# Optimization experiments

Measured on AMD Instinct MI355X. Metric: run time of the kernel, lower is better.

Reference implementation:

```python
import jax, jax.numpy as jnp
import numpy as np

B, S, H, E = 2, 4096, 2048, 8


def setup_inputs() -> dict:
    key = jax.random.key(0)
    k1, k2, k3 = jax.random.split(key, 3)
    x = jax.random.normal(k1, (B, S, H), dtype=jnp.float32)
    w_router = jax.random.normal(k2, (E, H), dtype=jnp.float32) * (1.0 / np.sqrt(H))
    # nn.Linear weight layout: [out_features, in_features] per expert -> [E, H, H]
    w_experts = jax.random.normal(k3, (E, H, H), dtype=jnp.float32) * (1.0 / np.sqrt(H))
    return {"x": x, "w_router": w_router, "w_experts": w_experts}


def reference(x, w_router, w_experts):
    # router logits: x @ W_r^T  -> [B, S, E]
    logits = jnp.einsum('bsh,eh->bse', x, w_router)
    idx = jnp.argmax(logits, axis=-1)  # [B, S] top-1 expert per token
    # dense all-expert outputs (matches original which evaluates every expert):
    # expert_e(x) = x @ W_e^T -> [B, S, E, H]
    all_out = jnp.einsum('bsh,efh->bsef', x, w_experts)
    # masked sum over one-hot mask == gather of the selected expert output
    out = jnp.take_along_axis(all_out, idx[:, :, None, None], axis=2)[:, :, 0, :]
    return out
```

## Files before the change

### kernel.cpp

```cpp
#include <hip/hip_runtime.h>
#include <hip/hip_bf16.h>
#include <cstdint>

#define T_TOK 8192
#define H_DIM 2048
#define N_EXP 8
#define FLAGBIT 0x80000000u

typedef __attribute__((ext_vector_type(4))) float f32x4;
typedef __attribute__((ext_vector_type(8))) short bf16x8;

__device__ __forceinline__ unsigned short f2bf(float f) {
  unsigned int u = __builtin_bit_cast(unsigned int, f);
  u += 0x7fffu + ((u >> 16) & 1u);
  return (unsigned short)(u >> 16);
}

#define GLL(SRC, DST) __builtin_amdgcn_global_load_lds( \
    (const __attribute__((address_space(1))) void*)(SRC), \
    (__attribute__((address_space(3))) void*)(DST), 16, 0, 0)

__global__ __launch_bounds__(256, 4) void k_conv_a(const float* __restrict__ we,
                                                   unsigned short* __restrict__ wb) {
  const size_t tix = ((size_t)blockIdx.x * 256 + threadIdx.x) * 8;
  const size_t stride = (size_t)1024 * 256 * 8;
  f32x4 v[16];
#pragma unroll
  for (int it = 0; it < 8; ++it) {
    v[2 * it]     = *reinterpret_cast<const f32x4*>(we + tix + (size_t)it * stride);
    v[2 * it + 1] = *reinterpret_cast<const f32x4*>(we + tix + (size_t)it * stride + 4);
  }
#pragma unroll
  for (int it = 0; it < 8; ++it) {
    union { unsigned short h[8]; uint4 u; } r;
#pragma unroll
    for (int q = 0; q < 4; ++q) {
      r.h[q]     = f2bf(v[2 * it][q]);
      r.h[4 + q] = f2bf(v[2 * it + 1][q]);
    }
    *reinterpret_cast<uint4*>(wb + tix + (size_t)it * stride) = r.u;
  }
}

__global__ __launch_bounds__(256, 4) void k_conv_b(const float* __restrict__ we,
                                                   unsigned short* __restrict__ wb) {
  const size_t tix = ((size_t)blockIdx.x * 256 + threadIdx.x) * 8;
  const size_t stride = (size_t)1024 * 256 * 8;
#pragma unroll
  for (int it = 0; it < 8; ++it) {
    const f32x4 a = *reinterpret_cast<const f32x4*>(we + tix + (size_t)it * stride);
    const f32x4 b = *reinterpret_cast<const f32x4*>(we + tix + (size_t)it * stride + 4);
    union { unsigned short h[8]; uint4 u; } r;
#pragma unroll
    for (int q = 0; q < 4; ++q) { r.h[q] = f2bf(a[q]); r.h[4 + q] = f2bf(b[q]); }
    *reinterpret_cast<uint4*>(wb + tix + (size_t)it * stride) = r.u;
  }
}

__global__ __launch_bounds__(256, 2) void k_router(const float* __restrict__ x,
    const float* __restrict__ wr, unsigned short* __restrict__ xb,
    int* __restrict__ idx)
{
  const int wv = threadIdx.x >> 6, lane = threadIdx.x & 63;
  const int t0 = (blockIdx.x * 4 + wv) * 4;
  float acc[4][N_EXP];
#pragma unroll
  for (int tt = 0; tt < 4; ++tt)
#pragma unroll
    for (int e = 0; e < N_EXP; ++e) acc[tt][e] = 0.f;
#pragma unroll
  for (int c = 0; c < H_DIM / 256; ++c) {
    const int h = c * 256 + lane * 4;
    float4 wvv[N_EXP];
#pragma unroll
    for (int e = 0; e < N_EXP; ++e)
      wvv[e] = *reinterpret_cast<const float4*>(wr + e * H_DIM + h);
#pragma unroll
    for (int tt = 0; tt < 4; ++tt) {
      const float4 xv = *reinterpret_cast<const float4*>(x + (size_t)(t0 + tt) * H_DIM + h);
      ushort4 bv;
      bv.x = f2bf(xv.x); bv.y = f2bf(xv.y); bv.z = f2bf(xv.z); bv.w = f2bf(xv.w);
      *reinterpret_cast<ushort4*>(xb + (size_t)(t0 + tt) * H_DIM + h) = bv;
#pragma unroll
      for (int e = 0; e < N_EXP; ++e) {
        acc[tt][e] = fmaf(xv.x, wvv[e].x, acc[tt][e]);
        acc[tt][e] = fmaf(xv.y, wvv[e].y, acc[tt][e]);
        acc[tt][e] = fmaf(xv.z, wvv[e].z, acc[tt][e]);
        acc[tt][e] = fmaf(xv.w, wvv[e].w, acc[tt][e]);
      }
    }
  }
#pragma unroll
  for (int off = 32; off >= 1; off >>= 1)
#pragma unroll
    for (int tt = 0; tt < 4; ++tt)
#pragma unroll
      for (int e = 0; e < N_EXP; ++e) acc[tt][e] += __shfl_xor(acc[tt][e], off, 64);
  if (lane == 0) {
#pragma unroll
    for (int tt = 0; tt < 4; ++tt) {
      float best = acc[tt][0]; int be = 0;
#pragma unroll
      for (int e = 1; e < N_EXP; ++e) if (acc[tt][e] > best) { best = acc[tt][e]; be = e; }
      idx[t0 + tt] = be;
    }
  }
}

__global__ __launch_bounds__(1024) void k_sort(const int* __restrict__ idx,
    int* __restrict__ tlist, int* __restrict__ estar, int* __restrict__ mlo,
    int* __restrict__ mhi, int* __restrict__ rpos, int* __restrict__ rtile,
    int* __restrict__ rtc)
{
  __shared__ int wc[N_EXP][128];
  __shared__ int wbase[N_EXP][128];
  __shared__ int sTot[N_EXP];
  __shared__ int off[N_EXP + 1];
  __shared__ int sE[32], sCnt[N_EXP], sBase[N_EXP];
  const int tid = threadIdx.x, w = tid >> 6, l = tid & 63;
  int myE[8];
#pragma unroll
  for (int j = 0; j < 8; ++j) {
    myE[j] = idx[j * 1024 + tid];
#pragma unroll
    for (int e = 0; e < N_EXP; ++e) {
      const unsigned long long bm = __ballot(myE[j] == e);
      if (l == e) wc[e][j * 16 + w] = __popcll(bm);
    }
  }
  __syncthreads();
  if (tid < N_EXP) {
    int s = 0;
    for (int k = 0; k < 128; ++k) { wbase[tid][k] = s; s += wc[tid][k]; }
    sTot[tid] = s;
  }
  __syncthreads();
  if (tid == 0) {
    off[0] = 0;
    for (int e = 0; e < N_EXP; ++e) off[e + 1] = off[e] + sTot[e];
  }
  __syncthreads();
#pragma unroll
  for (int j = 0; j < 8; ++j) {
    int rank = 0;
#pragma unroll
    for (int e = 0; e < N_EXP; ++e) {
      const unsigned long long bm = __ballot(myE[j] == e);
      if (myE[j] == e) rank = __popcll(bm & ((1ull << l) - 1ull));
    }
    tlist[off[myE[j]] + wbase[myE[j]][j * 16 + w] + rank] = j * 1024 + tid;
  }
  if (tid < 32) {
    const int lo = tid * 256, hi = lo + 256;
    int bl = -1, bE = 0, bLo = 0, bHi = 0;
#pragma unroll
    for (int e = 0; e < N_EXP; ++e) {
      const int a = off[e] > lo ? off[e] : lo;
      const int b = off[e + 1] < hi ? off[e + 1] : hi;
      if (b - a > bl) { bl = b - a; bE = e; bLo = a - lo; bHi = b - lo; }
    }
    sE[tid] = bE; estar[tid] = bE; mlo[tid] = bLo; mhi[tid] = bHi;
  }
  __syncthreads();
  if (tid < N_EXP) {
    int cnt = 0;
    for (int t = 0; t < 32; ++t) {
      if (sE[t] == tid) continue;
      const int lo = t * 256, hi = lo + 256;
      const int a = off[tid] > lo ? off[tid] : lo;
      const int b = off[tid + 1] < hi ? off[tid + 1] : hi;
      if (b > a) cnt += b - a;
    }
    sCnt[tid] = cnt;
  }
  __syncthreads();
  if (tid == 0) {
    int base = 0, ntile = 0;
    for (int e = 0; e < N_EXP; ++e) {
      sBase[e] = base;
      const int pt = (sCnt[e] + 127) >> 7;
      for (int k = 0; k < pt; ++k) rtile[ntile++] = e;
      base += pt << 7;
    }
    *rtc = ntile;
  }
  __syncthreads();
  if (tid < N_EXP && sCnt[tid] > 0) {
    int ptr = sBase[tid], firstp = -1;
    for (int t = 0; t < 32; ++t) {
      if (sE[t] == tid) continue;
      const int lo = t * 256, hi = lo + 256;
      const int a = off[tid] > lo ? off[tid] : lo;
      const int b = off[tid + 1] < hi ? off[tid + 1] : hi;
      for (int p = a; p < b; ++p) { if (firstp < 0) firstp = p; rpos[ptr++] = p; }
    }
    const int end = sBase[tid] + (((sCnt[tid] + 127) >> 7) << 7);
    for (; ptr < end; ++ptr) rpos[ptr] = (int)((unsigned)firstp | FLAGBIT);
  }
}

template<int Q, bool LOADB, bool VMC>
__device__ __forceinline__ void gphase(const char* LP,
    __attribute__((address_space(3))) char* LDS3,
    int rdBase, int aRowOff, int bRowOff, int ch0, int ch1,
    bf16x8 (&bfr)[8], f32x4 (&acc)[8][4],
    const unsigned short* s0, const unsigned short* s1, int d0, int d1)
{
  if constexpr (LOADB) {
#pragma unroll
    for (int nf = 0; nf < 4; ++nf) {
      bfr[nf * 2 + 0] = *reinterpret_cast<const bf16x8*>(LP + rdBase + 32768 + bRowOff + nf * 2048 + ch0);
      bfr[nf * 2 + 1] = *reinterpret_cast<const bf16x8*>(LP + rdBase + 32768 + bRowOff + nf * 2048 + ch1);
    }
  }
  bf16x8 af[2][2];
#pragma unroll
  for (int m = 0; m < 2; ++m) {
    af[m][0] = *reinterpret_cast<const bf16x8*>(LP + rdBase + aRowOff + (2 * Q + m) * 2048 + ch0);
    af[m][1] = *reinterpret_cast<const bf16x8*>(LP + rdBase + aRowOff + (2 * Q + m) * 2048 + ch1);
  }
  GLL(s0, LDS3 + d0);
  GLL(s1, LDS3 + d1);
  __builtin_amdgcn_sched_barrier(0);
  __builtin_amdgcn_s_barrier();
  __builtin_amdgcn_sched_barrier(0);
  __builtin_amdgcn_s_setprio(1);
#pragma unroll
  for (int ks = 0; ks < 2; ++ks)
#pragma unroll
    for (int m = 0; m < 2; ++m)
#pragma unroll
      for (int nf = 0; nf < 4; ++nf)
        acc[2 * Q + m][nf] = __builtin_amdgcn_mfma_f32_16x16x32_bf16(af[m][ks], bfr[nf * 2 + ks], acc[2 * Q + m][nf], 0, 0, 0);
  __builtin_amdgcn_s_setprio(0);
  if constexpr (VMC) asm volatile("s_waitcnt vmcnt(4)" ::: "memory");
  __builtin_amdgcn_sched_barrier(0);
  __builtin_amdgcn_s_barrier();
  __builtin_amdgcn_sched_barrier(0);
}

__global__ __launch_bounds__(512, 2) void k_gemm(const unsigned short* __restrict__ xb,
    const unsigned short* __restrict__ wb, const int* __restrict__ tlist,
    const int* __restrict__ estar, const int* __restrict__ mlo, const int* __restrict__ mhi,
    float* __restrict__ out)
{
  __shared__ short lds[65536];
  const int bid = blockIdx.x;
  const int mt = (bid & 7) * 4 + ((bid >> 3) & 3);
  const int nt = bid >> 5;
  const int m0 = mt * 256, f0 = nt * 256;
  const int e = estar[mt], mLo = mlo[mt], mHi = mhi[mt];
  const int tid = threadIdx.x;
  const int l = tid & 63, wv = tid >> 6;
  const int wm = wv >> 2, wn = wv & 3;
  const int l16 = l & 15, g = l >> 4;
  const char* LP = (const char*)lds;
  auto* LDS3 = (__attribute__((address_space(3))) char*)lds;

  const int sw = l16 & 7;
  const int ch0 = ((0 + g) ^ sw) << 4;
  const int ch1 = ((4 + g) ^ sw) << 4;
  const int aRowOff = (wm * 128 + l16) * 128;
  const int bRowOff = (wn * 64 + l16) * 128;

  const int csrc = ((l & 7) ^ ((l >> 3) & 7)) * 8;
  const int srow = l >> 3;
  const unsigned short* aP[2][2];
  const unsigned short* bP[2][2];
  const unsigned short* wpan = wb + (size_t)e * H_DIM * H_DIM;
#pragma unroll
  for (int h = 0; h < 2; ++h)
#pragma unroll
    for (int j = 0; j < 2; ++j) {
      const int tok = tlist[m0 + h * 128 + (wv * 2 + j) * 8 + srow];
      aP[h][j] = xb + (size_t)tok * H_DIM + csrc;
      bP[h][j] = wpan + (size_t)(f0 + h * 128 + (wv * 2 + j) * 8 + srow) * H_DIM + csrc;
    }
  const int sl0 = wv * 2048, sl1 = wv * 2048 + 1024;

  f32x4 acc[8][4];
#pragma unroll
  for (int mf = 0; mf < 8; ++mf)
#pragma unroll
    for (int nf = 0; nf < 4; ++nf) acc[mf][nf] = (f32x4){0.f, 0.f, 0.f, 0.f};
  bf16x8 bfr[8];

  GLL(aP[0][0], LDS3 + 0 + sl0);      GLL(aP[0][1], LDS3 + 0 + sl1);
  GLL(aP[1][0], LDS3 + 16384 + sl0);  GLL(aP[1][1], LDS3 + 16384 + sl1);
  GLL(bP[0][0], LDS3 + 32768 + sl0);  GLL(bP[0][1], LDS3 + 32768 + sl1);
  GLL(bP[1][0], LDS3 + 49152 + sl0);  GLL(bP[1][1], LDS3 + 49152 + sl1);
  GLL(bP[0][0] + 64, LDS3 + 65536 + 32768 + sl0);  GLL(bP[0][1] + 64, LDS3 + 65536 + 32768 + sl1);
  GLL(bP[1][0] + 64, LDS3 + 65536 + 49152 + sl0);  GLL(bP[1][1] + 64, LDS3 + 65536 + 49152 + sl1);
  asm volatile("s_waitcnt vmcnt(4)" ::: "memory");
  __builtin_amdgcn_sched_barrier(0);
  __builtin_amdgcn_s_barrier();
  __builtin_amdgcn_sched_barrier(0);

  for (int i = 0; i < 16; ++i) {
    const int kk1 = ((2 * i + 1) << 6) & (H_DIM - 1);
    const int kk2 = ((2 * i + 2) << 6) & (H_DIM - 1);
    const int kk3 = ((2 * i + 3) << 6) & (H_DIM - 1);
    gphase<0, true , false>(LP, LDS3, 0, aRowOff, bRowOff, ch0, ch1, bfr, acc,
        aP[0][0] + kk1, aP[0][1] + kk1, 65536 + 0 + sl0, 65536 + 0 + sl1);
    gphase<1, false, false>(LP, LDS3, 0, aRowOff, bRowOff, ch0, ch1, bfr, acc,
        aP[1][0] + kk1, aP[1][1] + kk1, 65536 + 16384 + sl0, 65536 + 16384 + sl1);
    gphase<2, false, false>(LP, LDS3, 0, aRowOff, bRowOff, ch0, ch1, bfr, acc,
        bP[0][0] + kk2, bP[0][1] + kk2, 0 + 32768 + sl0, 0 + 32768 + sl1);
    gphase<3, false, true >(LP, LDS3, 0, aRowOff, bRowOff, ch0, ch1, bfr, acc,
        bP[1][0] + kk2, bP[1][1] + kk2, 0 + 49152 + sl0, 0 + 49152 + sl1);
    gphase<0, true , false>(LP, LDS3, 65536, aRowOff, bRowOff, ch0, ch1, bfr, acc,
        aP[0][0] + kk2, aP[0][1] + kk2, 0 + 0 + sl0, 0 + 0 + sl1);
    gphase<1, false, false>(LP, LDS3, 65536, aRowOff, bRowOff, ch0, ch1, bfr, acc,
        aP[1][0] + kk2, aP[1][1] + kk2, 0 + 16384 + sl0, 0 + 16384 + sl1);
    gphase<2, false, false>(LP, LDS3, 65536, aRowOff, bRowOff, ch0, ch1, bfr, acc,
        bP[0][0] + kk3, bP[0][1] + kk3, 65536 + 32768 + sl0, 65536 + 32768 + sl1);
    gphase<3, false, true >(LP, LDS3, 65536, aRowOff, bRowOff, ch0, ch1, bfr, acc,
        bP[1][0] + kk3, bP[1][1] + kk3, 65536 + 49152 + sl0, 65536 + 49152 + sl1);
  }

#pragma unroll
  for (int mf = 0; mf < 8; ++mf) {
#pragma unroll
    for (int r = 0; r < 4; ++r) {
      const int row = wm * 128 + mf * 16 + g * 4 + r;
      const int t = tlist[m0 + row];
      const bool own = (row >= mLo) && (row < mHi);
      float* op = out + (size_t)t * H_DIM + f0 + wn * 64 + l16;
#pragma unroll
      for (int nf = 0; nf < 4; ++nf) op[nf * 16] = own ? acc[mf][nf][r] : 0.f;
    }
  }
}

__global__ __launch_bounds__(256, 2) void k_repair(const unsigned short* __restrict__ xb,
    const unsigned short* __restrict__ wb, const int* __restrict__ tlist,
    const int* __restrict__ rpos, const int* __restrict__ rtile, const int* __restrict__ rtc,
    float* __restrict__ out)
{
  const int bx = blockIdx.x;
  if (bx >= *rtc) return;
  __shared__ short lds[24576];
  const int f0 = blockIdx.y * 256, kc = blockIdx.z;
  const int e = rtile[bx];
  const int tid = threadIdx.x, l = tid & 63, wv = tid >> 6;
  const int wm = wv >> 1, wn = wv & 1;
  const int l16 = l & 15, g = l >> 4;
  const char* LP = (const char*)lds;
  auto* LDS3 = (__attribute__((address_space(3))) char*)lds;
  const int sw = l16 & 7;
  const int ch0 = ((0 + g) ^ sw) << 4, ch1 = ((4 + g) ^ sw) << 4;
  const int csrc = ((l & 7) ^ ((l >> 3) & 7)) * 8;
  const int srow = l >> 3;

  const unsigned short* aS[4];
#pragma unroll
  for (int j = 0; j < 4; ++j) {
    const int ent = rpos[bx * 128 + (wv * 4 + j) * 8 + srow];
    const int tok = tlist[ent & 0x7fffffff];
    aS[j] = xb + (size_t)tok * H_DIM + csrc;
  }
  const unsigned short* bS[8];
#pragma unroll
  for (int j = 0; j < 8; ++j)
    bS[j] = wb + (size_t)e * H_DIM * H_DIM + (size_t)(f0 + (wv * 8 + j) * 8 + srow) * H_DIM + csrc;

  f32x4 acc[4][8];
#pragma unroll
  for (int mf = 0; mf < 4; ++mf)
#pragma unroll
    for (int nf = 0; nf < 8; ++nf) acc[mf][nf] = (f32x4){0.f, 0.f, 0.f, 0.f};

  for (int it = 0; it < 8; ++it) {
    const int kk = kc * 512 + it * 64;
    __syncthreads();
#pragma unroll
    for (int j = 0; j < 4; ++j) GLL(aS[j] + kk, LDS3 + (wv * 4 + j) * 1024);
#pragma unroll
    for (int j = 0; j < 8; ++j) GLL(bS[j] + kk, LDS3 + 16384 + (wv * 8 + j) * 1024);
    __syncthreads();
    bf16x8 af[4][2];
#pragma unroll
    for (int mf = 0; mf < 4; ++mf) {
      af[mf][0] = *reinterpret_cast<const bf16x8*>(LP + (wm * 64 + mf * 16 + l16) * 128 + ch0);
      af[mf][1] = *reinterpret_cast<const bf16x8*>(LP + (wm * 64 + mf * 16 + l16) * 128 + ch1);
    }
#pragma unroll
    for (int nf = 0; nf < 8; ++nf) {
      const bf16x8 b0 = *reinterpret_cast<const bf16x8*>(LP + 16384 + (wn * 128 + nf * 16 + l16) * 128 + ch0);
      const bf16x8 b1 = *reinterpret_cast<const bf16x8*>(LP + 16384 + (wn * 128 + nf * 16 + l16) * 128 + ch1);
#pragma unroll
      for (int mf = 0; mf < 4; ++mf) {
        acc[mf][nf] = __builtin_amdgcn_mfma_f32_16x16x32_bf16(af[mf][0], b0, acc[mf][nf], 0, 0, 0);
        acc[mf][nf] = __builtin_amdgcn_mfma_f32_16x16x32_bf16(af[mf][1], b1, acc[mf][nf], 0, 0, 0);
      }
    }
  }
#pragma unroll
  for (int mf = 0; mf < 4; ++mf) {
#pragma unroll
    for (int r = 0; r < 4; ++r) {
      const int row = wm * 64 + mf * 16 + g * 4 + r;
      const int ent = rpos[bx * 128 + row];
      if (!((unsigned)ent & FLAGBIT)) {
        const int tok = tlist[ent];
        float* op = out + (size_t)tok * H_DIM + f0 + wn * 128 + l16;
#pragma unroll
        for (int nf = 0; nf < 8; ++nf) atomicAdd(op + nf * 16, acc[mf][nf][r]);
      }
    }
  }
}

extern "C" void kernel_launch(void* const* d_in, const int* in_sizes, int n_in,
                              void* d_out, int out_size, void* d_ws, size_t ws_size,
                              hipStream_t stream) {
  const float* x  = (const float*)d_in[0];
  const float* wr = (const float*)d_in[1];
  const float* we = (const float*)d_in[2];
  float* out = (float*)d_out;

  char* p = (char*)d_ws;
  unsigned short* xb = (unsigned short*)p; p += (size_t)T_TOK * H_DIM * 2;
  unsigned short* wb = (unsigned short*)p; p += (size_t)N_EXP * H_DIM * H_DIM * 2;
  int* idx    = (int*)p; p += T_TOK * 4;
  int* tlist  = (int*)p; p += T_TOK * 4;
  int* rpos   = (int*)p; p += T_TOK * 4;
  int* estar  = (int*)p; p += 32 * 4;
  int* mlo    = (int*)p; p += 32 * 4;
  int* mhi    = (int*)p; p += 32 * 4;
  int* rtile  = (int*)p; p += 64 * 4;
  int* rtc    = (int*)p; p += 64;

  const size_t half = (size_t)4 * H_DIM * H_DIM;
  k_conv_a<<<1024, 256, 0, stream>>>(we, wb);
  k_conv_b<<<1024, 256, 0, stream>>>(we + half, wb + half);
  k_router<<<512, 256, 0, stream>>>(x, wr, xb, idx);
  k_sort<<<1, 1024, 0, stream>>>(idx, tlist, estar, mlo, mhi, rpos, rtile, rtc);
  k_gemm<<<256, 512, 0, stream>>>(xb, wb, tlist, estar, mlo, mhi, out);
  k_repair<<<dim3(64, 8, 4), 256, 0, stream>>>(xb, wb, tlist, rpos, rtile, rtc, out);
}
```

Measured before the change: 208.4 us.

## Fuse fp32-to-bf16 expert weight conversion into grouped GEMM B-tile loading

Removes the two standalone weight conversion kernels and the bf16 weight workspace. The GEMM and repair kernels now read fp32 expert weights directly into registers, convert them with packed bf16 conversion instructions, and write the swizzled bf16 tiles to LDS, interleaved with the existing MFMA phases. This avoids converting all eight experts' weights up front and the extra write/read pass through HBM. In exchange the GEMM reads twice the bytes per B tile, uses more registers, and adds vmcnt(0)/lgkmcnt(0) waits that may stall the pipeline.

```diff
diff --git a/kernel.cpp b/kernel.cpp
--- a/kernel.cpp
+++ b/kernel.cpp
@@ -16,46 +16,21 @@
   return (unsigned short)(u >> 16);
 }
 
+__device__ __forceinline__ unsigned cvtpk(float lo, float hi) {
+  unsigned r;
+  asm("v_cvt_pk_bf16_f32 %0, %1, %2" : "=v"(r) : "v"(lo), "v"(hi));
+  return r;
+}
+__device__ __forceinline__ uint4 pk16(const f32x4& a, const f32x4& b) {
+  uint4 r;
+  r.x = cvtpk(a[0], a[1]); r.y = cvtpk(a[2], a[3]);
+  r.z = cvtpk(b[0], b[1]); r.w = cvtpk(b[2], b[3]);
+  return r;
+}
+
 #define GLL(SRC, DST) __builtin_amdgcn_global_load_lds( \
     (const __attribute__((address_space(1))) void*)(SRC), \
     (__attribute__((address_space(3))) void*)(DST), 16, 0, 0)
-
-__global__ __launch_bounds__(256, 4) void k_conv_a(const float* __restrict__ we,
-                                                   unsigned short* __restrict__ wb) {
-  const size_t tix = ((size_t)blockIdx.x * 256 + threadIdx.x) * 8;
-  const size_t stride = (size_t)1024 * 256 * 8;
-  f32x4 v[16];
-#pragma unroll
-  for (int it = 0; it < 8; ++it) {
-    v[2 * it]     = *reinterpret_cast<const f32x4*>(we + tix + (size_t)it * stride);
-    v[2 * it + 1] = *reinterpret_cast<const f32x4*>(we + tix + (size_t)it * stride + 4);
-  }
-#pragma unroll
-  for (int it = 0; it < 8; ++it) {
-    union { unsigned short h[8]; uint4 u; } r;
-#pragma unroll
-    for (int q = 0; q < 4; ++q) {
-      r.h[q]     = f2bf(v[2 * it][q]);
-      r.h[4 + q] = f2bf(v[2 * it + 1][q]);
-    }
-    *reinterpret_cast<uint4*>(wb + tix + (size_t)it * stride) = r.u;
-  }
-}
-
-__global__ __launch_bounds__(256, 4) void k_conv_b(const float* __restrict__ we,
-                                                   unsigned short* __restrict__ wb) {
-  const size_t tix = ((size_t)blockIdx.x * 256 + threadIdx.x) * 8;
-  const size_t stride = (size_t)1024 * 256 * 8;
-#pragma unroll
-  for (int it = 0; it < 8; ++it) {
-    const f32x4 a = *reinterpret_cast<const f32x4*>(we + tix + (size_t)it * stride);
-    const f32x4 b = *reinterpret_cast<const f32x4*>(we + tix + (size_t)it * stride + 4);
-    union { unsigned short h[8]; uint4 u; } r;
-#pragma unroll
-    for (int q = 0; q < 4; ++q) { r.h[q] = f2bf(a[q]); r.h[4 + q] = f2bf(b[q]); }
-    *reinterpret_cast<uint4*>(wb + tix + (size_t)it * stride) = r.u;
-  }
-}
 
 __global__ __launch_bounds__(256, 2) void k_router(const float* __restrict__ x,
     const float* __restrict__ wr, unsigned short* __restrict__ xb,
@@ -199,14 +174,22 @@
   }
 }
 
-template<int Q, bool LOADB, bool VMC>
-__device__ __forceinline__ void gphase(const char* LP,
+template<int Q, bool FULL, bool VMC0>
+__device__ __forceinline__ void gphase(const char* LP, char* LW,
     __attribute__((address_space(3))) char* LDS3,
     int rdBase, int aRowOff, int bRowOff, int ch0, int ch1,
-    bf16x8 (&bfr)[8], f32x4 (&acc)[8][4],
-    const unsigned short* s0, const unsigned short* s1, int d0, int d1)
+    bf16x8 (&bfr)[8], f32x4 (&acc)[8][4], f32x4 (&bv)[8], uint4 (&bw)[4],
+    const unsigned short* a00, const unsigned short* a01,
+    const unsigned short* a10, const unsigned short* a11,
+    const float* bF0, const float* bF1, int kkB,
+    int sl0, int sl1, int wO0, int wO1, int wO2, int wO3)
 {
-  if constexpr (LOADB) {
+  const int dstO = rdBase ^ 65536;
+  if constexpr (FULL) {
+    *reinterpret_cast<uint4*>(LW + dstO + wO0) = bw[0];
+    *reinterpret_cast<uint4*>(LW + dstO + wO1) = bw[1];
+    *reinterpret_cast<uint4*>(LW + dstO + wO2) = bw[2];
+    *reinterpret_cast<uint4*>(LW + dstO + wO3) = bw[3];
 #pragma unroll
     for (int nf = 0; nf < 4; ++nf) {
       bfr[nf * 2 + 0] = *reinterpret_cast<const bf16x8*>(LP + rdBase + 32768 + bRowOff + nf * 2048 + ch0);
@@ -219,8 +202,20 @@
     af[m][0] = *reinterpret_cast<const bf16x8*>(LP + rdBase + aRowOff + (2 * Q + m) * 2048 + ch0);
     af[m][1] = *reinterpret_cast<const bf16x8*>(LP + rdBase + aRowOff + (2 * Q + m) * 2048 + ch1);
   }
-  GLL(s0, LDS3 + d0);
-  GLL(s1, LDS3 + d1);
+  if constexpr (FULL) {
+    bv[0] = *reinterpret_cast<const f32x4*>(bF0 + kkB);
+    bv[1] = *reinterpret_cast<const f32x4*>(bF0 + kkB + 4);
+    bv[2] = *reinterpret_cast<const f32x4*>(bF0 + kkB + 8);
+    bv[3] = *reinterpret_cast<const f32x4*>(bF0 + kkB + 12);
+    bv[4] = *reinterpret_cast<const f32x4*>(bF1 + kkB);
+    bv[5] = *reinterpret_cast<const f32x4*>(bF1 + kkB + 4);
+    bv[6] = *reinterpret_cast<const f32x4*>(bF1 + kkB + 8);
+    bv[7] = *reinterpret_cast<const f32x4*>(bF1 + kkB + 12);
+    GLL(a00, LDS3 + dstO + 0 + sl0);
+    GLL(a01, LDS3 + dstO + 0 + sl1);
+    GLL(a10, LDS3 + dstO + 16384 + sl0);
+    GLL(a11, LDS3 + dstO + 16384 + sl1);
+  }
   __builtin_amdgcn_sched_barrier(0);
   __builtin_amdgcn_s_barrier();
   __builtin_amdgcn_sched_barrier(0);
@@ -233,14 +228,21 @@
       for (int nf = 0; nf < 4; ++nf)
         acc[2 * Q + m][nf] = __builtin_amdgcn_mfma_f32_16x16x32_bf16(af[m][ks], bfr[nf * 2 + ks], acc[2 * Q + m][nf], 0, 0, 0);
   __builtin_amdgcn_s_setprio(0);
-  if constexpr (VMC) asm volatile("s_waitcnt vmcnt(4)" ::: "memory");
+  if constexpr (VMC0) {
+    asm volatile("s_waitcnt vmcnt(0)" ::: "memory");
+    bw[0] = pk16(bv[0], bv[1]); bw[1] = pk16(bv[2], bv[3]);
+    bw[2] = pk16(bv[4], bv[5]); bw[3] = pk16(bv[6], bv[7]);
+  }
+  if constexpr (FULL) {
+    asm volatile("s_waitcnt lgkmcnt(0)" ::: "memory");
+  }
   __builtin_amdgcn_sched_barrier(0);
   __builtin_amdgcn_s_barrier();
   __builtin_amdgcn_sched_barrier(0);
 }
 
 __global__ __launch_bounds__(512, 2) void k_gemm(const unsigned short* __restrict__ xb,
-    const unsigned short* __restrict__ wb, const int* __restrict__ tlist,
+    const float* __restrict__ we, const int* __restrict__ tlist,
     const int* __restrict__ estar, const int* __restrict__ mlo, const int* __restrict__ mhi,
     float* __restrict__ out)
 {
@@ -255,6 +257,7 @@
   const int wm = wv >> 2, wn = wv & 3;
   const int l16 = l & 15, g = l >> 4;
   const char* LP = (const char*)lds;
+  char* LW = (char*)lds;
   auto* LDS3 = (__attribute__((address_space(3))) char*)lds;
 
   const int sw = l16 & 7;
@@ -265,18 +268,28 @@
 
   const int csrc = ((l & 7) ^ ((l >> 3) & 7)) * 8;
   const int srow = l >> 3;
-  const unsigned short* aP[2][2];
-  const unsigned short* bP[2][2];
-  const unsigned short* wpan = wb + (size_t)e * H_DIM * H_DIM;
-#pragma unroll
-  for (int h = 0; h < 2; ++h)
-#pragma unroll
-    for (int j = 0; j < 2; ++j) {
-      const int tok = tlist[m0 + h * 128 + (wv * 2 + j) * 8 + srow];
-      aP[h][j] = xb + (size_t)tok * H_DIM + csrc;
-      bP[h][j] = wpan + (size_t)(f0 + h * 128 + (wv * 2 + j) * 8 + srow) * H_DIM + csrc;
-    }
+  const unsigned short *a00, *a01, *a10, *a11;
+  {
+    const int t00 = tlist[m0 + 0 * 128 + (wv * 2 + 0) * 8 + srow];
+    const int t01 = tlist[m0 + 0 * 128 + (wv * 2 + 1) * 8 + srow];
+    const int t10 = tlist[m0 + 1 * 128 + (wv * 2 + 0) * 8 + srow];
+    const int t11 = tlist[m0 + 1 * 128 + (wv * 2 + 1) * 8 + srow];
+    a00 = xb + (size_t)t00 * H_DIM + csrc;
+    a01 = xb + (size_t)t01 * H_DIM + csrc;
+    a10 = xb + (size_t)t10 * H_DIM + csrc;
+    a11 = xb + (size_t)t11 * H_DIM + csrc;
+  }
   const int sl0 = wv * 2048, sl1 = wv * 2048 + 1024;
+
+  const int rB = tid >> 2;
+  const int cB = (tid & 3) * 16;
+  const float* bF0 = we + (size_t)e * H_DIM * H_DIM + (size_t)(f0 + rB) * H_DIM + cB;
+  const float* bF1 = bF0 + (size_t)128 * H_DIM;
+  const int s0c = 2 * (tid & 3), rk = rB & 7;
+  const int wO0 = 32768 + rB * 128 + ((s0c ^ rk) << 4);
+  const int wO1 = 32768 + rB * 128 + (((s0c + 1) ^ rk) << 4);
+  const int wO2 = wO0 + 16384;
+  const int wO3 = wO1 + 16384;
 
   f32x4 acc[8][4];
 #pragma unroll
@@ -284,38 +297,55 @@
 #pragma unroll
     for (int nf = 0; nf < 4; ++nf) acc[mf][nf] = (f32x4){0.f, 0.f, 0.f, 0.f};
   bf16x8 bfr[8];
-
-  GLL(aP[0][0], LDS3 + 0 + sl0);      GLL(aP[0][1], LDS3 + 0 + sl1);
-  GLL(aP[1][0], LDS3 + 16384 + sl0);  GLL(aP[1][1], LDS3 + 16384 + sl1);
-  GLL(bP[0][0], LDS3 + 32768 + sl0);  GLL(bP[0][1], LDS3 + 32768 + sl1);
-  GLL(bP[1][0], LDS3 + 49152 + sl0);  GLL(bP[1][1], LDS3 + 49152 + sl1);
-  GLL(bP[0][0] + 64, LDS3 + 65536 + 32768 + sl0);  GLL(bP[0][1] + 64, LDS3 + 65536 + 32768 + sl1);
-  GLL(bP[1][0] + 64, LDS3 + 65536 + 49152 + sl0);  GLL(bP[1][1] + 64, LDS3 + 65536 + 49152 + sl1);
-  asm volatile("s_waitcnt vmcnt(4)" ::: "memory");
+  f32x4 bv[8];
+  uint4 bw[4];
+
+  bv[0] = *reinterpret_cast<const f32x4*>(bF0);      bv[1] = *reinterpret_cast<const f32x4*>(bF0 + 4);
+  bv[2] = *reinterpret_cast<const f32x4*>(bF0 + 8);  bv[3] = *reinterpret_cast<const f32x4*>(bF0 + 12);
+  bv[4] = *reinterpret_cast<const f32x4*>(bF1);      bv[5] = *reinterpret_cast<const f32x4*>(bF1 + 4);
+  bv[6] = *reinterpret_cast<const f32x4*>(bF1 + 8);  bv[7] = *reinterpret_cast<const f32x4*>(bF1 + 12);
+  bw[0] = pk16(bv[0], bv[1]); bw[1] = pk16(bv[2], bv[3]);
+  bw[2] = pk16(bv[4], bv[5]); bw[3] = pk16(bv[6], bv[7]);
+  *reinterpret_cast<uint4*>(LW + wO0) = bw[0];
+  *reinterpret_cast<uint4*>(LW + wO1) = bw[1];
+  *reinterpret_cast<uint4*>(LW + wO2) = bw[2];
+  *reinterpret_cast<uint4*>(LW + wO3) = bw[3];
+  bv[0] = *reinterpret_cast<const f32x4*>(bF0 + 64);      bv[1] = *reinterpret_cast<const f32x4*>(bF0 + 68);
+  bv[2] = *reinterpret_cast<const f32x4*>(bF0 + 72);      bv[3] = *reinterpret_cast<const f32x4*>(bF0 + 76);
+  bv[4] = *reinterpret_cast<const f32x4*>(bF1 + 64);      bv[5] = *reinterpret_cast<const f32x4*>(bF1 + 68);
+  bv[6] = *reinterpret_cast<const f32x4*>(bF1 + 72);      bv[7] = *reinterpret_cast<const f32x4*>(bF1 + 76);
+  GLL(a00, LDS3 + 0 + sl0);
+  GLL(a01, LDS3 + 0 + sl1);
+  GLL(a10, LDS3 + 16384 + sl0);
+  GLL(a11, LDS3 + 16384 + sl1);
+  bw[0] = pk16(bv[0], bv[1]); bw[1] = pk16(bv[2], bv[3]);
+  bw[2] = pk16(bv[4], bv[5]); bw[3] = pk16(bv[6], bv[7]);
+  asm volatile("s_waitcnt vmcnt(0)" ::: "memory");
+  asm volatile("s_waitcnt lgkmcnt(0)" ::: "memory");
   __builtin_amdgcn_sched_barrier(0);
   __builtin_amdgcn_s_barrier();
   __builtin_amdgcn_sched_barrier(0);
 
   for (int i = 0; i < 16; ++i) {
-    const int kk1 = ((2 * i + 1) << 6) & (H_DIM - 1);
+    const int kk1 = (2 * i + 1) << 6;
     const int kk2 = ((2 * i + 2) << 6) & (H_DIM - 1);
     const int kk3 = ((2 * i + 3) << 6) & (H_DIM - 1);
-    gphase<0, true , false>(LP, LDS3, 0, aRowOff, bRowOff, ch0, ch1, bfr, acc,
-        aP[0][0] + kk1, aP[0][1] + kk1, 65536 + 0 + sl0, 65536 + 0 + sl1);
-    gphase<1, false, false>(LP, LDS3, 0, aRowOff, bRowOff, ch0, ch1, bfr, acc,
-        aP[1][0] + kk1, aP[1][1] + kk1, 65536 + 16384 + sl0, 65536 + 16384 + sl1);
-    gphase<2, false, false>(LP, LDS3, 0, aRowOff, bRowOff, ch0, ch1, bfr, acc,
-        bP[0][0] + kk2, bP[0][1] + kk2, 0 + 32768 + sl0, 0 + 32768 + sl1);
-    gphase<3, false, true >(LP, LDS3, 0, aRowOff, bRowOff, ch0, ch1, bfr, acc,
-        bP[1][0] + kk2, bP[1][1] + kk2, 0 + 49152 + sl0, 0 + 49152 + sl1);
-    gphase<0, true , false>(LP, LDS3, 65536, aRowOff, bRowOff, ch0, ch1, bfr, acc,
-        aP[0][0] + kk2, aP[0][1] + kk2, 0 + 0 + sl0, 0 + 0 + sl1);
-    gphase<1, false, false>(LP, LDS3, 65536, aRowOff, bRowOff, ch0, ch1, bfr, acc,
-        aP[1][0] + kk2, aP[1][1] + kk2, 0 + 16384 + sl0, 0 + 16384 + sl1);
-    gphase<2, false, false>(LP, LDS3, 65536, aRowOff, bRowOff, ch0, ch1, bfr, acc,
-        bP[0][0] + kk3, bP[0][1] + kk3, 65536 + 32768 + sl0, 65536 + 32768 + sl1);
-    gphase<3, false, true >(LP, LDS3, 65536, aRowOff, bRowOff, ch0, ch1, bfr, acc,
-        bP[1][0] + kk3, bP[1][1] + kk3, 65536 + 49152 + sl0, 65536 + 49152 + sl1);
+    gphase<0, true , false>(LP, LW, LDS3, 0, aRowOff, bRowOff, ch0, ch1, bfr, acc, bv, bw,
+        a00 + kk1, a01 + kk1, a10 + kk1, a11 + kk1, bF0, bF1, kk2, sl0, sl1, wO0, wO1, wO2, wO3);
+    gphase<1, false, false>(LP, LW, LDS3, 0, aRowOff, bRowOff, ch0, ch1, bfr, acc, bv, bw,
+        a00, a01, a10, a11, bF0, bF1, 0, sl0, sl1, wO0, wO1, wO2, wO3);
+    gphase<2, false, false>(LP, LW, LDS3, 0, aRowOff, bRowOff, ch0, ch1, bfr, acc, bv, bw,
+        a00, a01, a10, a11, bF0, bF1, 0, sl0, sl1, wO0, wO1, wO2, wO3);
+    gphase<3, false, true >(LP, LW, LDS3, 0, aRowOff, bRowOff, ch0, ch1, bfr, acc, bv, bw,
+        a00, a01, a10, a11, bF0, bF1, 0, sl0, sl1, wO0, wO1, wO2, wO3);
+    gphase<0, true , false>(LP, LW, LDS3, 65536, aRowOff, bRowOff, ch0, ch1, bfr, acc, bv, bw,
+        a00 + kk2, a01 + kk2, a10 + kk2, a11 + kk2, bF0, bF1, kk3, sl0, sl1, wO0, wO1, wO2, wO3);
+    gphase<1, false, false>(LP, LW, LDS3, 65536, aRowOff, bRowOff, ch0, ch1, bfr, acc, bv, bw,
+        a00, a01, a10, a11, bF0, bF1, 0, sl0, sl1, wO0, wO1, wO2, wO3);
+    gphase<2, false, false>(LP, LW, LDS3, 65536, aRowOff, bRowOff, ch0, ch1, bfr, acc, bv, bw,
+        a00, a01, a10, a11, bF0, bF1, 0, sl0, sl1, wO0, wO1, wO2, wO3);
+    gphase<3, false, true >(LP, LW, LDS3, 65536, aRowOff, bRowOff, ch0, ch1, bfr, acc, bv, bw,
+        a00, a01, a10, a11, bF0, bF1, 0, sl0, sl1, wO0, wO1, wO2, wO3);
   }
 
 #pragma unroll
@@ -333,7 +363,7 @@
 }
 
 __global__ __launch_bounds__(256, 2) void k_repair(const unsigned short* __restrict__ xb,
-    const unsigned short* __restrict__ wb, const int* __restrict__ tlist,
+    const float* __restrict__ we, const int* __restrict__ tlist,
     const int* __restrict__ rpos, const int* __restrict__ rtile, const int* __restrict__ rtc,
     float* __restrict__ out)
 {
@@ -346,6 +376,7 @@
   const int wm = wv >> 1, wn = wv & 1;
   const int l16 = l & 15, g = l >> 4;
   const char* LP = (const char*)lds;
+  char* LW = (char*)lds;
   auto* LDS3 = (__attribute__((address_space(3))) char*)lds;
   const int sw = l16 & 7;
   const int ch0 = ((0 + g) ^ sw) << 4, ch1 = ((4 + g) ^ sw) << 4;
@@ -359,10 +390,9 @@
     const int tok = tlist[ent & 0x7fffffff];
     aS[j] = xb + (size_t)tok * H_DIM + csrc;
   }
-  const unsigned short* bS[8];
-#pragma unroll
-  for (int j = 0; j < 8; ++j)
-    bS[j] = wb + (size_t)e * H_DIM * H_DIM + (size_t)(f0 + (wv * 8 + j) * 8 + srow) * H_DIM + csrc;
+  const int rR = tid >> 3, sR = tid & 7;
+  const int swO = 16384 + rR * 128 + ((sR ^ (rR & 7)) << 4);
+  const float* bFr = we + (size_t)e * H_DIM * H_DIM + (size_t)(f0 + rR) * H_DIM + sR * 8;
 
   f32x4 acc[4][8];
 #pragma unroll
@@ -375,8 +405,16 @@
     __syncthreads();
 #pragma unroll
     for (int j = 0; j < 4; ++j) GLL(aS[j] + kk, LDS3 + (wv * 4 + j) * 1024);
-#pragma unroll
-    for (int j = 0; j < 8; ++j) GLL(bS[j] + kk, LDS3 + 16384 + (wv * 8 + j) * 1024);
+    f32x4 bv[16];
+#pragma unroll
+    for (int j = 0; j < 8; ++j) {
+      const float* s = bFr + (size_t)(32 * j) * H_DIM + kk;
+      bv[2 * j]     = *reinterpret_cast<const f32x4*>(s);
+      bv[2 * j + 1] = *reinterpret_cast<const f32x4*>(s + 4);
+    }
+#pragma unroll
+    for (int j = 0; j < 8; ++j)
+      *reinterpret_cast<uint4*>(LW + swO + j * 4096) = pk16(bv[2 * j], bv[2 * j + 1]);
     __syncthreads();
     bf16x8 af[4][2];
 #pragma unroll
@@ -421,7 +459,6 @@
 
   char* p = (char*)d_ws;
   unsigned short* xb = (unsigned short*)p; p += (size_t)T_TOK * H_DIM * 2;
-  unsigned short* wb = (unsigned short*)p; p += (size_t)N_EXP * H_DIM * H_DIM * 2;
   int* idx    = (int*)p; p += T_TOK * 4;
   int* tlist  = (int*)p; p += T_TOK * 4;
   int* rpos   = (int*)p; p += T_TOK * 4;
@@ -431,11 +468,8 @@
   int* rtile  = (int*)p; p += 64 * 4;
   int* rtc    = (int*)p; p += 64;
 
-  const size_t half = (size_t)4 * H_DIM * H_DIM;
-  k_conv_a<<<1024, 256, 0, stream>>>(we, wb);
-  k_conv_b<<<1024, 256, 0, stream>>>(we + half, wb + half);
   k_router<<<512, 256, 0, stream>>>(x, wr, xb, idx);
   k_sort<<<1, 1024, 0, stream>>>(idx, tlist, estar, mlo, mhi, rpos, rtile, rtc);
-  k_gemm<<<256, 512, 0, stream>>>(xb, wb, tlist, estar, mlo, mhi, out);
-  k_repair<<<dim3(64, 8, 4), 256, 0, stream>>>(xb, wb, tlist, rpos, rtile, rtc, out);
-}
+  k_gemm<<<256, 512, 0, stream>>>(xb, we, tlist, estar, mlo, mhi, out);
+  k_repair<<<dim3(64, 8, 4), 256, 0, stream>>>(xb, we, tlist, rpos, rtile, rtc, out);
+}
```

Measured after the change: 252.6 us. +21.2%, slower.

## Fuse conversion and router kernels; merge repair into GEMM launch without atomics

Applied to the files above, without the earlier changes.

Merges the two weight-conversion kernels and the router into one launch, with blocks split by index, and gives the router one token per wave. The repair GEMM becomes extra blocks inside the main GEMM launch, using the full K range and a 4-way N split. Its outputs are written with plain stores instead of split-K atomics, and main-GEMM rows that are not owned are skipped rather than zero-written. This removes three kernel launches and the atomic traffic, at the cost of less parallelism in the repair path and repair blocks sharing the grid with main tiles.

```diff
diff --git a/kernel.cpp b/kernel.cpp
--- a/kernel.cpp
+++ b/kernel.cpp
@@ -20,90 +20,57 @@
     (const __attribute__((address_space(1))) void*)(SRC), \
     (__attribute__((address_space(3))) void*)(DST), 16, 0, 0)
 
-__global__ __launch_bounds__(256, 4) void k_conv_a(const float* __restrict__ we,
-                                                   unsigned short* __restrict__ wb) {
-  const size_t tix = ((size_t)blockIdx.x * 256 + threadIdx.x) * 8;
-  const size_t stride = (size_t)1024 * 256 * 8;
-  f32x4 v[16];
-#pragma unroll
-  for (int it = 0; it < 8; ++it) {
-    v[2 * it]     = *reinterpret_cast<const f32x4*>(we + tix + (size_t)it * stride);
-    v[2 * it + 1] = *reinterpret_cast<const f32x4*>(we + tix + (size_t)it * stride + 4);
-  }
-#pragma unroll
-  for (int it = 0; it < 8; ++it) {
-    union { unsigned short h[8]; uint4 u; } r;
-#pragma unroll
-    for (int q = 0; q < 4; ++q) {
-      r.h[q]     = f2bf(v[2 * it][q]);
-      r.h[4 + q] = f2bf(v[2 * it + 1][q]);
-    }
-    *reinterpret_cast<uint4*>(wb + tix + (size_t)it * stride) = r.u;
-  }
-}
-
-__global__ __launch_bounds__(256, 4) void k_conv_b(const float* __restrict__ we,
-                                                   unsigned short* __restrict__ wb) {
-  const size_t tix = ((size_t)blockIdx.x * 256 + threadIdx.x) * 8;
-  const size_t stride = (size_t)1024 * 256 * 8;
-#pragma unroll
-  for (int it = 0; it < 8; ++it) {
-    const f32x4 a = *reinterpret_cast<const f32x4*>(we + tix + (size_t)it * stride);
-    const f32x4 b = *reinterpret_cast<const f32x4*>(we + tix + (size_t)it * stride + 4);
-    union { unsigned short h[8]; uint4 u; } r;
-#pragma unroll
-    for (int q = 0; q < 4; ++q) { r.h[q] = f2bf(a[q]); r.h[4 + q] = f2bf(b[q]); }
-    *reinterpret_cast<uint4*>(wb + tix + (size_t)it * stride) = r.u;
-  }
-}
-
-__global__ __launch_bounds__(256, 2) void k_router(const float* __restrict__ x,
-    const float* __restrict__ wr, unsigned short* __restrict__ xb,
+__global__ __launch_bounds__(256, 4) void k_pre(const float* __restrict__ x,
+    const float* __restrict__ wr, const float* __restrict__ we,
+    unsigned short* __restrict__ xb, unsigned short* __restrict__ wb,
     int* __restrict__ idx)
 {
+  const int bid = blockIdx.x;
+  if (bid < 4096) {
+    const size_t tix = ((size_t)bid * 256 + threadIdx.x) * 8;
+    const size_t stride = (size_t)4096 * 256 * 8;
+#pragma unroll
+    for (int it = 0; it < 4; ++it) {
+      const f32x4 a = *reinterpret_cast<const f32x4*>(we + tix + (size_t)it * stride);
+      const f32x4 b = *reinterpret_cast<const f32x4*>(we + tix + (size_t)it * stride + 4);
+      union { unsigned short h[8]; uint4 u; } r;
+#pragma unroll
+      for (int q = 0; q < 4; ++q) { r.h[q] = f2bf(a[q]); r.h[4 + q] = f2bf(b[q]); }
+      *reinterpret_cast<uint4*>(wb + tix + (size_t)it * stride) = r.u;
+    }
+    return;
+  }
   const int wv = threadIdx.x >> 6, lane = threadIdx.x & 63;
-  const int t0 = (blockIdx.x * 4 + wv) * 4;
-  float acc[4][N_EXP];
-#pragma unroll
-  for (int tt = 0; tt < 4; ++tt)
-#pragma unroll
-    for (int e = 0; e < N_EXP; ++e) acc[tt][e] = 0.f;
+  const int t = (bid - 4096) * 4 + wv;
+  const float* xp = x + (size_t)t * H_DIM;
+  float acc[N_EXP];
+#pragma unroll
+  for (int e = 0; e < N_EXP; ++e) acc[e] = 0.f;
 #pragma unroll
   for (int c = 0; c < H_DIM / 256; ++c) {
     const int h = c * 256 + lane * 4;
-    float4 wvv[N_EXP];
-#pragma unroll
-    for (int e = 0; e < N_EXP; ++e)
-      wvv[e] = *reinterpret_cast<const float4*>(wr + e * H_DIM + h);
-#pragma unroll
-    for (int tt = 0; tt < 4; ++tt) {
-      const float4 xv = *reinterpret_cast<const float4*>(x + (size_t)(t0 + tt) * H_DIM + h);
-      ushort4 bv;
-      bv.x = f2bf(xv.x); bv.y = f2bf(xv.y); bv.z = f2bf(xv.z); bv.w = f2bf(xv.w);
-      *reinterpret_cast<ushort4*>(xb + (size_t)(t0 + tt) * H_DIM + h) = bv;
-#pragma unroll
-      for (int e = 0; e < N_EXP; ++e) {
-        acc[tt][e] = fmaf(xv.x, wvv[e].x, acc[tt][e]);
-        acc[tt][e] = fmaf(xv.y, wvv[e].y, acc[tt][e]);
-        acc[tt][e] = fmaf(xv.z, wvv[e].z, acc[tt][e]);
-        acc[tt][e] = fmaf(xv.w, wvv[e].w, acc[tt][e]);
-      }
+    const float4 xv = *reinterpret_cast<const float4*>(xp + h);
+    ushort4 bv;
+    bv.x = f2bf(xv.x); bv.y = f2bf(xv.y); bv.z = f2bf(xv.z); bv.w = f2bf(xv.w);
+    *reinterpret_cast<ushort4*>(xb + (size_t)t * H_DIM + h) = bv;
+#pragma unroll
+    for (int e = 0; e < N_EXP; ++e) {
+      const float4 wv4 = *reinterpret_cast<const float4*>(wr + e * H_DIM + h);
+      acc[e] = fmaf(xv.x, wv4.x, acc[e]);
+      acc[e] = fmaf(xv.y, wv4.y, acc[e]);
+      acc[e] = fmaf(xv.z, wv4.z, acc[e]);
+      acc[e] = fmaf(xv.w, wv4.w, acc[e]);
     }
   }
 #pragma unroll
   for (int off = 32; off >= 1; off >>= 1)
 #pragma unroll
-    for (int tt = 0; tt < 4; ++tt)
-#pragma unroll
-      for (int e = 0; e < N_EXP; ++e) acc[tt][e] += __shfl_xor(acc[tt][e], off, 64);
+    for (int e = 0; e < N_EXP; ++e) acc[e] += __shfl_xor(acc[e], off, 64);
   if (lane == 0) {
-#pragma unroll
-    for (int tt = 0; tt < 4; ++tt) {
-      float best = acc[tt][0]; int be = 0;
-#pragma unroll
-      for (int e = 1; e < N_EXP; ++e) if (acc[tt][e] > best) { best = acc[tt][e]; be = e; }
-      idx[t0 + tt] = be;
-    }
+    float best = acc[0]; int be = 0;
+#pragma unroll
+    for (int e = 1; e < N_EXP; ++e) if (acc[e] > best) { best = acc[e]; be = e; }
+    idx[t] = be;
   }
 }
 
@@ -242,141 +209,132 @@
 __global__ __launch_bounds__(512, 2) void k_gemm(const unsigned short* __restrict__ xb,
     const unsigned short* __restrict__ wb, const int* __restrict__ tlist,
     const int* __restrict__ estar, const int* __restrict__ mlo, const int* __restrict__ mhi,
+    const int* __restrict__ rpos, const int* __restrict__ rtile, const int* __restrict__ rtc,
     float* __restrict__ out)
 {
   __shared__ short lds[65536];
   const int bid = blockIdx.x;
-  const int mt = (bid & 7) * 4 + ((bid >> 3) & 3);
-  const int nt = bid >> 5;
-  const int m0 = mt * 256, f0 = nt * 256;
-  const int e = estar[mt], mLo = mlo[mt], mHi = mhi[mt];
   const int tid = threadIdx.x;
   const int l = tid & 63, wv = tid >> 6;
-  const int wm = wv >> 2, wn = wv & 3;
-  const int l16 = l & 15, g = l >> 4;
-  const char* LP = (const char*)lds;
-  auto* LDS3 = (__attribute__((address_space(3))) char*)lds;
-
-  const int sw = l16 & 7;
-  const int ch0 = ((0 + g) ^ sw) << 4;
-  const int ch1 = ((4 + g) ^ sw) << 4;
-  const int aRowOff = (wm * 128 + l16) * 128;
-  const int bRowOff = (wn * 64 + l16) * 128;
-
-  const int csrc = ((l & 7) ^ ((l >> 3) & 7)) * 8;
-  const int srow = l >> 3;
-  const unsigned short* aP[2][2];
-  const unsigned short* bP[2][2];
-  const unsigned short* wpan = wb + (size_t)e * H_DIM * H_DIM;
-#pragma unroll
-  for (int h = 0; h < 2; ++h)
-#pragma unroll
-    for (int j = 0; j < 2; ++j) {
-      const int tok = tlist[m0 + h * 128 + (wv * 2 + j) * 8 + srow];
-      aP[h][j] = xb + (size_t)tok * H_DIM + csrc;
-      bP[h][j] = wpan + (size_t)(f0 + h * 128 + (wv * 2 + j) * 8 + srow) * H_DIM + csrc;
-    }
-  const int sl0 = wv * 2048, sl1 = wv * 2048 + 1024;
-
-  f32x4 acc[8][4];
-#pragma unroll
-  for (int mf = 0; mf < 8; ++mf)
-#pragma unroll
-    for (int nf = 0; nf < 4; ++nf) acc[mf][nf] = (f32x4){0.f, 0.f, 0.f, 0.f};
-  bf16x8 bfr[8];
-
-  GLL(aP[0][0], LDS3 + 0 + sl0);      GLL(aP[0][1], LDS3 + 0 + sl1);
-  GLL(aP[1][0], LDS3 + 16384 + sl0);  GLL(aP[1][1], LDS3 + 16384 + sl1);
-  GLL(bP[0][0], LDS3 + 32768 + sl0);  GLL(bP[0][1], LDS3 + 32768 + sl1);
-  GLL(bP[1][0], LDS3 + 49152 + sl0);  GLL(bP[1][1], LDS3 + 49152 + sl1);
-  GLL(bP[0][0] + 64, LDS3 + 65536 + 32768 + sl0);  GLL(bP[0][1] + 64, LDS3 + 65536 + 32768 + sl1);
-  GLL(bP[1][0] + 64, LDS3 + 65536 + 49152 + sl0);  GLL(bP[1][1] + 64, LDS3 + 65536 + 49152 + sl1);
-  asm volatile("s_waitcnt vmcnt(4)" ::: "memory");
-  __builtin_amdgcn_sched_barrier(0);
-  __builtin_amdgcn_s_barrier();
-  __builtin_amdgcn_sched_barrier(0);
-
-  for (int i = 0; i < 16; ++i) {
-    const int kk1 = ((2 * i + 1) << 6) & (H_DIM - 1);
-    const int kk2 = ((2 * i + 2) << 6) & (H_DIM - 1);
-    const int kk3 = ((2 * i + 3) << 6) & (H_DIM - 1);
-    gphase<0, true , false>(LP, LDS3, 0, aRowOff, bRowOff, ch0, ch1, bfr, acc,
-        aP[0][0] + kk1, aP[0][1] + kk1, 65536 + 0 + sl0, 65536 + 0 + sl1);
-    gphase<1, false, false>(LP, LDS3, 0, aRowOff, bRowOff, ch0, ch1, bfr, acc,
-        aP[1][0] + kk1, aP[1][1] + kk1, 65536 + 16384 + sl0, 65536 + 16384 + sl1);
-    gphase<2, false, false>(LP, LDS3, 0, aRowOff, bRowOff, ch0, ch1, bfr, acc,
-        bP[0][0] + kk2, bP[0][1] + kk2, 0 + 32768 + sl0, 0 + 32768 + sl1);
-    gphase<3, false, true >(LP, LDS3, 0, aRowOff, bRowOff, ch0, ch1, bfr, acc,
-        bP[1][0] + kk2, bP[1][1] + kk2, 0 + 49152 + sl0, 0 + 49152 + sl1);
-    gphase<0, true , false>(LP, LDS3, 65536, aRowOff, bRowOff, ch0, ch1, bfr, acc,
-        aP[0][0] + kk2, aP[0][1] + kk2, 0 + 0 + sl0, 0 + 0 + sl1);
-    gphase<1, false, false>(LP, LDS3, 65536, aRowOff, bRowOff, ch0, ch1, bfr, acc,
-        aP[1][0] + kk2, aP[1][1] + kk2, 0 + 16384 + sl0, 0 + 16384 + sl1);
-    gphase<2, false, false>(LP, LDS3, 65536, aRowOff, bRowOff, ch0, ch1, bfr, acc,
-        bP[0][0] + kk3, bP[0][1] + kk3, 65536 + 32768 + sl0, 65536 + 32768 + sl1);
-    gphase<3, false, true >(LP, LDS3, 65536, aRowOff, bRowOff, ch0, ch1, bfr, acc,
-        bP[1][0] + kk3, bP[1][1] + kk3, 65536 + 49152 + sl0, 65536 + 49152 + sl1);
-  }
-
-#pragma unroll
-  for (int mf = 0; mf < 8; ++mf) {
-#pragma unroll
-    for (int r = 0; r < 4; ++r) {
-      const int row = wm * 128 + mf * 16 + g * 4 + r;
-      const int t = tlist[m0 + row];
-      const bool own = (row >= mLo) && (row < mHi);
-      float* op = out + (size_t)t * H_DIM + f0 + wn * 64 + l16;
-#pragma unroll
-      for (int nf = 0; nf < 4; ++nf) op[nf * 16] = own ? acc[mf][nf][r] : 0.f;
-    }
-  }
-}
-
-__global__ __launch_bounds__(256, 2) void k_repair(const unsigned short* __restrict__ xb,
-    const unsigned short* __restrict__ wb, const int* __restrict__ tlist,
-    const int* __restrict__ rpos, const int* __restrict__ rtile, const int* __restrict__ rtc,
-    float* __restrict__ out)
-{
-  const int bx = blockIdx.x;
-  if (bx >= *rtc) return;
-  __shared__ short lds[24576];
-  const int f0 = blockIdx.y * 256, kc = blockIdx.z;
-  const int e = rtile[bx];
-  const int tid = threadIdx.x, l = tid & 63, wv = tid >> 6;
-  const int wm = wv >> 1, wn = wv & 1;
   const int l16 = l & 15, g = l >> 4;
   const char* LP = (const char*)lds;
   auto* LDS3 = (__attribute__((address_space(3))) char*)lds;
   const int sw = l16 & 7;
-  const int ch0 = ((0 + g) ^ sw) << 4, ch1 = ((4 + g) ^ sw) << 4;
+  const int ch0 = ((0 + g) ^ sw) << 4;
+  const int ch1 = ((4 + g) ^ sw) << 4;
   const int csrc = ((l & 7) ^ ((l >> 3) & 7)) * 8;
   const int srow = l >> 3;
 
-  const unsigned short* aS[4];
-#pragma unroll
-  for (int j = 0; j < 4; ++j) {
-    const int ent = rpos[bx * 128 + (wv * 4 + j) * 8 + srow];
+  if (bid < 256) {
+    const int mt = (bid & 7) * 4 + ((bid >> 3) & 3);
+    const int nt = bid >> 5;
+    const int m0 = mt * 256, f0 = nt * 256;
+    const int e = estar[mt], mLo = mlo[mt], mHi = mhi[mt];
+    const int wm = wv >> 2, wn = wv & 3;
+    const int aRowOff = (wm * 128 + l16) * 128;
+    const int bRowOff = (wn * 64 + l16) * 128;
+
+    const unsigned short* aP[2][2];
+    const unsigned short* bP[2][2];
+    const unsigned short* wpan = wb + (size_t)e * H_DIM * H_DIM;
+#pragma unroll
+    for (int h = 0; h < 2; ++h)
+#pragma unroll
+      for (int j = 0; j < 2; ++j) {
+        const int tok = tlist[m0 + h * 128 + (wv * 2 + j) * 8 + srow];
+        aP[h][j] = xb + (size_t)tok * H_DIM + csrc;
+        bP[h][j] = wpan + (size_t)(f0 + h * 128 + (wv * 2 + j) * 8 + srow) * H_DIM + csrc;
+      }
+    const int sl0 = wv * 2048, sl1 = wv * 2048 + 1024;
+
+    f32x4 acc[8][4];
+#pragma unroll
+    for (int mf = 0; mf < 8; ++mf)
+#pragma unroll
+      for (int nf = 0; nf < 4; ++nf) acc[mf][nf] = (f32x4){0.f, 0.f, 0.f, 0.f};
+    bf16x8 bfr[8];
+
+    GLL(aP[0][0], LDS3 + 0 + sl0);      GLL(aP[0][1], LDS3 + 0 + sl1);
+    GLL(aP[1][0], LDS3 + 16384 + sl0);  GLL(aP[1][1], LDS3 + 16384 + sl1);
+    GLL(bP[0][0], LDS3 + 32768 + sl0);  GLL(bP[0][1], LDS3 + 32768 + sl1);
+    GLL(bP[1][0], LDS3 + 49152 + sl0);  GLL(bP[1][1], LDS3 + 49152 + sl1);
+    GLL(bP[0][0] + 64, LDS3 + 65536 + 32768 + sl0);  GLL(bP[0][1] + 64, LDS3 + 65536 + 32768 + sl1);
+    GLL(bP[1][0] + 64, LDS3 + 65536 + 49152 + sl0);  GLL(bP[1][1] + 64, LDS3 + 65536 + 49152 + sl1);
+    asm volatile("s_waitcnt vmcnt(4)" ::: "memory");
+    __builtin_amdgcn_sched_barrier(0);
+    __builtin_amdgcn_s_barrier();
+    __builtin_amdgcn_sched_barrier(0);
+
+    for (int i = 0; i < 16; ++i) {
+      const int kk1 = ((2 * i + 1) << 6) & (H_DIM - 1);
+      const int kk2 = ((2 * i + 2) << 6) & (H_DIM - 1);
+      const int kk3 = ((2 * i + 3) << 6) & (H_DIM - 1);
+      gphase<0, true , false>(LP, LDS3, 0, aRowOff, bRowOff, ch0, ch1, bfr, acc,
+          aP[0][0] + kk1, aP[0][1] + kk1, 65536 + 0 + sl0, 65536 + 0 + sl1);
+      gphase<1, false, false>(LP, LDS3, 0, aRowOff, bRowOff, ch0, ch1, bfr, acc,
+          aP[1][0] + kk1, aP[1][1] + kk1, 65536 + 16384 + sl0, 65536 + 16384 + sl1);
+      gphase<2, false, false>(LP, LDS3, 0, aRowOff, bRowOff, ch0, ch1, bfr, acc,
+          bP[0][0] + kk2, bP[0][1] + kk2, 0 + 32768 + sl0, 0 + 32768 + sl1);
+      gphase<3, false, true >(LP, LDS3, 0, aRowOff, bRowOff, ch0, ch1, bfr, acc,
+          bP[1][0] + kk2, bP[1][1] + kk2, 0 + 49152 + sl0, 0 + 49152 + sl1);
+      gphase<0, true , false>(LP, LDS3, 65536, aRowOff, bRowOff, ch0, ch1, bfr, acc,
+          aP[0][0] + kk2, aP[0][1] + kk2, 0 + 0 + sl0, 0 + 0 + sl1);
+      gphase<1, false, false>(LP, LDS3, 65536, aRowOff, bRowOff, ch0, ch1, bfr, acc,
+          aP[1][0] + kk2, aP[1][1] + kk2, 0 + 16384 + sl0, 0 + 16384 + sl1);
+      gphase<2, false, false>(LP, LDS3, 65536, aRowOff, bRowOff, ch0, ch1, bfr, acc,
+          bP[0][0] + kk3, bP[0][1] + kk3, 65536 + 32768 + sl0, 65536 + 32768 + sl1);
+      gphase<3, false, true >(LP, LDS3, 65536, aRowOff, bRowOff, ch0, ch1, bfr, acc,
+          bP[1][0] + kk3, bP[1][1] + kk3, 65536 + 49152 + sl0, 65536 + 49152 + sl1);
+    }
+
+#pragma unroll
+    for (int mf = 0; mf < 8; ++mf) {
+#pragma unroll
+      for (int r = 0; r < 4; ++r) {
+        const int row = wm * 128 + mf * 16 + g * 4 + r;
+        if (row >= mLo && row < mHi) {
+          const int t = tlist[m0 + row];
+          float* op = out + (size_t)t * H_DIM + f0 + wn * 64 + l16;
+#pragma unroll
+          for (int nf = 0; nf < 4; ++nf) op[nf * 16] = acc[mf][nf][r];
+        }
+      }
+    }
+    return;
+  }
+
+  const int bid2 = bid - 256;
+  const int bx = bid2 >> 3;
+  if (bx >= *rtc) return;
+  const int f0 = (bid2 & 7) * 256;
+  const int e = rtile[bx];
+  const int wm = wv >> 2, wn = wv & 3;
+
+  const unsigned short* aS[2];
+#pragma unroll
+  for (int j = 0; j < 2; ++j) {
+    const int ent = rpos[bx * 128 + (wv * 2 + j) * 8 + srow];
     const int tok = tlist[ent & 0x7fffffff];
     aS[j] = xb + (size_t)tok * H_DIM + csrc;
   }
-  const unsigned short* bS[8];
-#pragma unroll
-  for (int j = 0; j < 8; ++j)
-    bS[j] = wb + (size_t)e * H_DIM * H_DIM + (size_t)(f0 + (wv * 8 + j) * 8 + srow) * H_DIM + csrc;
-
-  f32x4 acc[4][8];
+  const unsigned short* bS[4];
+#pragma unroll
+  for (int j = 0; j < 4; ++j)
+    bS[j] = wb + (size_t)e * H_DIM * H_DIM + (size_t)(f0 + (wv * 4 + j) * 8 + srow) * H_DIM + csrc;
+
+  f32x4 acc[4][4];
 #pragma unroll
   for (int mf = 0; mf < 4; ++mf)
 #pragma unroll
-    for (int nf = 0; nf < 8; ++nf) acc[mf][nf] = (f32x4){0.f, 0.f, 0.f, 0.f};
-
-  for (int it = 0; it < 8; ++it) {
-    const int kk = kc * 512 + it * 64;
+    for (int nf = 0; nf < 4; ++nf) acc[mf][nf] = (f32x4){0.f, 0.f, 0.f, 0.f};
+
+  for (int it = 0; it < 32; ++it) {
+    const int kk = it * 64;
     __syncthreads();
 #pragma unroll
-    for (int j = 0; j < 4; ++j) GLL(aS[j] + kk, LDS3 + (wv * 4 + j) * 1024);
-#pragma unroll
-    for (int j = 0; j < 8; ++j) GLL(bS[j] + kk, LDS3 + 16384 + (wv * 8 + j) * 1024);
+    for (int j = 0; j < 2; ++j) GLL(aS[j] + kk, LDS3 + (wv * 2 + j) * 1024);
+#pragma unroll
+    for (int j = 0; j < 4; ++j) GLL(bS[j] + kk, LDS3 + 16384 + (wv * 4 + j) * 1024);
     __syncthreads();
     bf16x8 af[4][2];
 #pragma unroll
@@ -385,9 +343,9 @@
       af[mf][1] = *reinterpret_cast<const bf16x8*>(LP + (wm * 64 + mf * 16 + l16) * 128 + ch1);
     }
 #pragma unroll
-    for (int nf = 0; nf < 8; ++nf) {
-      const bf16x8 b0 = *reinterpret_cast<const bf16x8*>(LP + 16384 + (wn * 128 + nf * 16 + l16) * 128 + ch0);
-      const bf16x8 b1 = *reinterpret_cast<const bf16x8*>(LP + 16384 + (wn * 128 + nf * 16 + l16) * 128 + ch1);
+    for (int nf = 0; nf < 4; ++nf) {
+      const bf16x8 b0 = *reinterpret_cast<const bf16x8*>(LP + 16384 + (wn * 64 + nf * 16 + l16) * 128 + ch0);
+      const bf16x8 b1 = *reinterpret_cast<const bf16x8*>(LP + 16384 + (wn * 64 + nf * 16 + l16) * 128 + ch1);
 #pragma unroll
       for (int mf = 0; mf < 4; ++mf) {
         acc[mf][nf] = __builtin_amdgcn_mfma_f32_16x16x32_bf16(af[mf][0], b0, acc[mf][nf], 0, 0, 0);
@@ -403,9 +361,9 @@
       const int ent = rpos[bx * 128 + row];
       if (!((unsigned)ent & FLAGBIT)) {
         const int tok = tlist[ent];
-        float* op = out + (size_t)tok * H_DIM + f0 + wn * 128 + l16;
-#pragma unroll
-        for (int nf = 0; nf < 8; ++nf) atomicAdd(op + nf * 16, acc[mf][nf][r]);
+        float* op = out + (size_t)tok * H_DIM + f0 + wn * 64 + l16;
+#pragma unroll
+        for (int nf = 0; nf < 4; ++nf) op[nf * 16] = acc[mf][nf][r];
       }
     }
   }
@@ -431,11 +389,7 @@
   int* rtile  = (int*)p; p += 64 * 4;
   int* rtc    = (int*)p; p += 64;
 
-  const size_t half = (size_t)4 * H_DIM * H_DIM;
-  k_conv_a<<<1024, 256, 0, stream>>>(we, wb);
-  k_conv_b<<<1024, 256, 0, stream>>>(we + half, wb + half);
-  k_router<<<512, 256, 0, stream>>>(x, wr, xb, idx);
+  k_pre<<<4096 + 2048, 256, 0, stream>>>(x, wr, we, xb, wb, idx);
   k_sort<<<1, 1024, 0, stream>>>(idx, tlist, estar, mlo, mhi, rpos, rtile, rtc);
-  k_gemm<<<256, 512, 0, stream>>>(xb, wb, tlist, estar, mlo, mhi, out);
-  k_repair<<<dim3(64, 8, 4), 256, 0, stream>>>(xb, wb, tlist, rpos, rtile, rtc, out);
-}
+  k_gemm<<<768, 512, 0, stream>>>(xb, wb, tlist, estar, mlo, mhi, rpos, rtile, rtc, out);
+}
```

Result: faster. 199.6 us (-4.2%).
